# Optimization experiments

Hardware: AMD Instinct MI355X
Metric: run time of the kernel (lower is better)

## Reference

```python
import jax, jax.numpy as jnp
import numpy as np

T, B, D = 512, 16, 2048


def setup_inputs() -> dict:
    key = jax.random.key(0)
    k1, k2, k3, k4, k5 = jax.random.split(key, 5)
    scale = 1.0 / np.sqrt(D)  # keep tanh pre-activations in a sane range
    return {
        "h0": jax.random.normal(k1, (B, D), dtype=jnp.float32),
        "x": jax.random.normal(k2, (T, B, D), dtype=jnp.float32),
        "Wx": jax.random.normal(k3, (D, D), dtype=jnp.float32) * scale,
        "Wh": jax.random.normal(k4, (D, D), dtype=jnp.float32) * scale,
        "Wo": jax.random.normal(k5, (D, D), dtype=jnp.float32) * scale,
    }


def reference(h0, x, Wx, Wh, Wo):
    # ONNX Scan with 1 state var, 1 scan input (axis 0, forward direction),
    # 1 scan output (stacked on axis 0, forward direction), 3 outer vars.
    # Body: h' = tanh(x_t @ Wx + h @ Wh); y_t = h' @ Wo
    def step(h, x_t):
        h_new = jnp.tanh(x_t @ Wx + h @ Wh)   # [B, D]
        y_t = h_new @ Wo                      # [B, D]
        return h_new, y_t

    h_final, ys = jax.lax.scan(step, h0, x)   # ys: [T, B, D]
    return (h_final, ys)
```

## Files before the change

### kernel.cpp

```cpp
#include <hip/hip_runtime.h>
#include <hip/hip_bf16.h>

#define DD 2048
#define TT 512
#define NBLK 64
#define HF_SLOT 32768
#define KT 64
#define SENT32 0x7FC07FC0u

typedef __attribute__((ext_vector_type(4))) float  f32x4;
typedef __attribute__((ext_vector_type(8))) short  bf16x8;
typedef __attribute__((ext_vector_type(8))) unsigned short u16x8;
typedef unsigned short ushort_t;
typedef unsigned long long u64_t;

__device__ __forceinline__ void gld_lds16(const void* g, void* l) {
    __builtin_amdgcn_global_load_lds(
        (const __attribute__((address_space(1))) unsigned int*)g,
        (__attribute__((address_space(3))) unsigned int*)l, 16, 0, 0);
}

__device__ __forceinline__ ushort_t f2bf(float v) {
    __hip_bfloat16 h = __float2bfloat16(v);
    return *(ushort_t*)&h;
}

__device__ __forceinline__ u64_t llc_load64(const u64_t* p) {
    return __hip_atomic_load(p, __ATOMIC_RELAXED, __HIP_MEMORY_SCOPE_AGENT);
}
__device__ __forceinline__ void llc_store64(u64_t* p, u64_t v) {
    __hip_atomic_store(p, v, __ATOMIC_RELAXED, __HIP_MEMORY_SCOPE_AGENT);
}
__device__ __forceinline__ float llc_loadf(const float* p) {
    return __hip_atomic_load(p, __ATOMIC_RELAXED, __HIP_MEMORY_SCOPE_AGENT);
}

__global__ void conv_frag(const float* __restrict__ src, ushort_t* __restrict__ dst) {
    int id = blockIdx.x * 256 + threadIdx.x;
    int l  = id & 63;
    int sk = (id >> 6) & 63;
    int mt = id >> 12;
    const float* s = src + (size_t)(mt * 16 + (l & 15)) * DD + sk * 32 + ((l >> 4) * 8);
    float4 a = *(const float4*)s;
    float4 b = *(const float4*)(s + 4);
    u16x8 r;
    r[0] = f2bf(a.x); r[1] = f2bf(a.y); r[2] = f2bf(a.z); r[3] = f2bf(a.w);
    r[4] = f2bf(b.x); r[5] = f2bf(b.y); r[6] = f2bf(b.z); r[7] = f2bf(b.w);
    *(u16x8*)(dst + (size_t)id * 8) = r;
}

__global__ void conv_wt(const float* __restrict__ W, ushort_t* __restrict__ Wt) {
    int id = blockIdx.x * 256 + threadIdx.x;
    int n  = id & (DD - 1);
    int k8 = id >> 11;
    u16x8 r;
#pragma unroll
    for (int j = 0; j < 8; ++j)
        r[j] = f2bf(W[(size_t)(k8 * 8 + j) * DD + n]);
    *(u16x8*)(Wt + (size_t)n * DD + k8 * 8) = r;
}

__global__ void fill_sent(u64_t* __restrict__ dst) {
    size_t id = (size_t)blockIdx.x * 256 + threadIdx.x;
    u64_t v = 0x7FC07FC07FC07FC0ull;
    dst[id * 2]     = v;
    dst[id * 2 + 1] = v;
}

__global__ __launch_bounds__(256) void gemm_frag(
    const ushort_t* __restrict__ Af, const ushort_t* __restrict__ Bt,
    float* __restrict__ C) {
    __shared__ ushort_t lA[8 * 64 * 8];
    __shared__ ushort_t lB[8 * 64 * 8];
    int tid = threadIdx.x;
    int w = tid >> 6, l = tid & 63;
    int wm = w >> 1, wn = w & 1;
    int quad = l >> 4, col = l & 15;
    int mt0 = blockIdx.x * 8;
    int n0  = blockIdx.y * 128;

    f32x4 acc[4][4] = {};

    for (int sk = 0; sk < KT; ++sk) {
        __syncthreads();
#pragma unroll
        for (int q = 0; q < 2; ++q) {
            int i = w * 2 + q;
            const ushort_t* ga = Af + ((size_t)((mt0 + i) * 64 + sk) * 64 + l) * 8;
            gld_lds16(ga, &lA[i * 512]);
            int jt = i;
            const ushort_t* gb = Bt + (size_t)(n0 + jt * 16 + col) * DD + sk * 32 + quad * 8;
            gld_lds16(gb, &lB[jt * 512]);
        }
        __syncthreads();
        bf16x8 af[4], bf[4];
#pragma unroll
        for (int i = 0; i < 4; ++i) af[i] = *(const bf16x8*)&lA[((wm * 4 + i) * 64 + l) * 8];
#pragma unroll
        for (int j = 0; j < 4; ++j) bf[j] = *(const bf16x8*)&lB[((wn * 4 + j) * 64 + l) * 8];
#pragma unroll
        for (int i = 0; i < 4; ++i)
#pragma unroll
            for (int j = 0; j < 4; ++j)
                acc[i][j] = __builtin_amdgcn_mfma_f32_16x16x32_bf16(af[i], bf[j], acc[i][j], 0, 0, 0);
    }

#pragma unroll
    for (int i = 0; i < 4; ++i)
#pragma unroll
        for (int j = 0; j < 4; ++j) {
            int rg0 = (mt0 + wm * 4 + i) * 16 + quad * 4;
            int cg  = n0 + (wn * 4 + j) * 16 + col;
#pragma unroll
            for (int r = 0; r < 4; ++r)
                C[(size_t)(rg0 + r) * DD + cg] = acc[i][j][r];
        }
}

__global__ __launch_bounds__(256, 1) void rnn_fused(
    const ushort_t* __restrict__ Wht,
    const ushort_t* __restrict__ Wot,
    ushort_t* __restrict__ Hf,
    const float* __restrict__ A32,
    float* __restrict__ out) {
    __shared__ ushort_t lW[4 * 16 * 2 * 512];
    __shared__ float scr[2048];
    __shared__ ushort_t hstage[512];
    int tid = threadIdx.x;
    int w = tid >> 6, l = tid & 63;
    int quad = l >> 4, col = l & 15;
    bool is_rnn = blockIdx.x < NBLK;
    int b = is_rnn ? blockIdx.x : blockIdx.x - NBLK;
    int c0 = b * 32;
    float* ys = out + HF_SLOT;

    const ushort_t* Wsrc = is_rnn ? Wht : Wot;
#pragma unroll
    for (int s = 0; s < 16; ++s) {
        int sk = w * 16 + s;
#pragma unroll
        for (int jt = 0; jt < 2; ++jt) {
            const ushort_t* gb = Wsrc + (size_t)(c0 + jt * 16 + col) * DD + sk * 32 + quad * 8;
            gld_lds16(gb, &lW[((sk * 2 + jt) << 9)]);
        }
    }
    __syncthreads();

    for (int t = 1; t <= TT; ++t) {
        float av[4];
        if (is_rnn && w < 2) {
#pragma unroll
            for (int r = 0; r < 4; ++r)
                av[r] = llc_loadf(&A32[(size_t)((t - 1) * 16 + quad * 4 + r) * DD + c0 + w * 16 + col]);
        }

        const ushort_t* hsrc = Hf + (size_t)(is_rnn ? t - 1 : t) * HF_SLOT;
        const u64_t* hbase = (const u64_t*)hsrc + ((size_t)(w * 16) * 64 + l) * 2;

        f32x4 acc0 = {0.f, 0.f, 0.f, 0.f};
        f32x4 acc1 = {0.f, 0.f, 0.f, 0.f};
        unsigned pend = 0xFFFFu;
        while (pend) {
            u64_t q0[16], q1[16];
#pragma unroll
            for (int s = 0; s < 16; ++s)
                if (pend & (1u << s)) {
                    const u64_t* p = hbase + (size_t)s * 128;
                    q0[s] = llc_load64(p);
                    q1[s] = llc_load64(p + 1);
                }
#pragma unroll
            for (int s = 0; s < 16; ++s)
                if (pend & (1u << s)) {
                    unsigned x0 = (unsigned)q0[s], x1 = (unsigned)(q0[s] >> 32);
                    unsigned x2 = (unsigned)q1[s], x3 = (unsigned)(q1[s] >> 32);
                    bool ok = (x0 != SENT32) & (x1 != SENT32) & (x2 != SENT32) & (x3 != SENT32);
                    if (__all((int)ok)) {
                        pend &= ~(1u << s);
                        union { u64_t q[2]; bf16x8 v; } u;
                        u.q[0] = q0[s]; u.q[1] = q1[s];
                        int sk = w * 16 + s;
                        bf16x8 w0 = *(const bf16x8*)&lW[((sk * 2 + 0) << 9) + l * 8];
                        bf16x8 w1 = *(const bf16x8*)&lW[((sk * 2 + 1) << 9) + l * 8];
                        acc0 = __builtin_amdgcn_mfma_f32_16x16x32_bf16(u.v, w0, acc0, 0, 0, 0);
                        acc1 = __builtin_amdgcn_mfma_f32_16x16x32_bf16(u.v, w1, acc1, 0, 0, 0);
                    }
                }
        }

        *(f32x4*)&scr[((w * 2 + 0) * 64 + l) * 4] = acc0;
        *(f32x4*)&scr[((w * 2 + 1) * 64 + l) * 4] = acc1;
        __syncthreads();

        if (w < 2) {
            int jt = w;
            f32x4 p0 = *(f32x4*)&scr[((0 * 2 + jt) * 64 + l) * 4];
            f32x4 p1 = *(f32x4*)&scr[((1 * 2 + jt) * 64 + l) * 4];
            f32x4 p2 = *(f32x4*)&scr[((2 * 2 + jt) * 64 + l) * 4];
            f32x4 p3 = *(f32x4*)&scr[((3 * 2 + jt) * 64 + l) * 4];
            int lc = jt * 16 + col;
            if (is_rnn) {
                int q2 = lc >> 3, jj = lc & 7;
#pragma unroll
                for (int r = 0; r < 4; ++r) {
                    int m = quad * 4 + r;
                    float x = p0[r] + p1[r] + p2[r] + p3[r] + av[r];
                    float e2 = __expf(-2.f * fabsf(x));
                    float th = copysignf((1.f - e2) / (1.f + e2), x);
                    hstage[(q2 * 16 + m) * 8 + jj] = f2bf(th);
                    if (t == TT) out[(size_t)m * DD + c0 + lc] = th;
                }
            } else {
#pragma unroll
                for (int r = 0; r < 4; ++r) {
                    int m = quad * 4 + r;
                    float y = p0[r] + p1[r] + p2[r] + p3[r];
                    ys[(size_t)((t - 1) * 16 + m) * DD + c0 + lc] = y;
                }
            }
        }

        __syncthreads();

        if (is_rnn && w == 0) {
            u64_t* dst = (u64_t*)(Hf + (size_t)t * HF_SLOT + (size_t)(c0 >> 5) * 512);
            const u64_t* sp = (const u64_t*)hstage;
            llc_store64(dst + l,      sp[l]);
            llc_store64(dst + 64 + l, sp[64 + l]);
        }
    }
}

extern "C" void kernel_launch(void* const* d_in, const int* in_sizes, int n_in,
                              void* d_out, int out_size, void* d_ws, size_t ws_size,
                              hipStream_t stream) {
    const float* h0 = (const float*)d_in[0];
    const float* x  = (const float*)d_in[1];
    const float* Wx = (const float*)d_in[2];
    const float* Wh = (const float*)d_in[3];
    const float* Wo = (const float*)d_in[4];
    float* out = (float*)d_out;

    char* ws = (char*)d_ws;
    ushort_t* Hf  = (ushort_t*)(ws + 4096);
    ushort_t* Xf  = Hf + HF_SLOT;
    size_t hf_bytes = (size_t)(TT + 1) * HF_SLOT * 2;
    ushort_t* Wxt = (ushort_t*)(ws + 4096 + hf_bytes);
    ushort_t* Wht = Wxt + (size_t)DD * DD;
    ushort_t* Wot = Wht + (size_t)DD * DD;
    float* A32 = out + HF_SLOT;

    conv_frag<<<8192, 256, 0, stream>>>(x, Xf);
    conv_frag<<<16, 256, 0, stream>>>(h0, Hf);
    conv_wt<<<2048, 256, 0, stream>>>(Wx, Wxt);
    conv_wt<<<2048, 256, 0, stream>>>(Wh, Wht);
    conv_wt<<<2048, 256, 0, stream>>>(Wo, Wot);

    gemm_frag<<<dim3(64, 16), 256, 0, stream>>>(Xf, Wxt, A32);

    fill_sent<<<8192, 256, 0, stream>>>((u64_t*)(Hf + HF_SLOT));

    rnn_fused<<<2 * NBLK, 256, 0, stream>>>(Wht, Wot, Hf, A32, out);
}
```

Baseline: 2.377 ms.

## Add per-block step flags to gate hidden-state polling and split MFMA accumulators

Adds a per-block progress flag array in the workspace. Each consumer wave spins on one 32-bit flag per source block until it reaches the needed step, and only then issues the sentinel-checked loads of the hidden state. The hidden-state publish moves into the tanh waves right after staging, which drops one barrier-ordered store phase, and the flag store follows it. The MFMA accumulation is split into two independent chains per output tile to shorten the dependency chain. Flag polling adds extra atomic traffic, and the relaxed ordering between the data stores and the flag store relies on the sentinel checks that are still in place.

```diff
diff --git a/kernel.cpp b/kernel.cpp
--- a/kernel.cpp
+++ b/kernel.cpp
@@ -6,6 +6,7 @@
 #define NBLK 64
 #define HF_SLOT 32768
 #define KT 64
+#define FSTRIDE 16
 #define SENT32 0x7FC07FC0u
 
 typedef __attribute__((ext_vector_type(4))) float  f32x4;
@@ -30,6 +31,9 @@
 }
 __device__ __forceinline__ void llc_store64(u64_t* p, u64_t v) {
     __hip_atomic_store(p, v, __ATOMIC_RELAXED, __HIP_MEMORY_SCOPE_AGENT);
+}
+__device__ __forceinline__ unsigned llc_load32(const unsigned* p) {
+    return __hip_atomic_load(p, __ATOMIC_RELAXED, __HIP_MEMORY_SCOPE_AGENT);
 }
 __device__ __forceinline__ float llc_loadf(const float* p) {
     return __hip_atomic_load(p, __ATOMIC_RELAXED, __HIP_MEMORY_SCOPE_AGENT);
@@ -122,7 +126,8 @@
     const ushort_t* __restrict__ Wot,
     ushort_t* __restrict__ Hf,
     const float* __restrict__ A32,
-    float* __restrict__ out) {
+    float* __restrict__ out,
+    unsigned* __restrict__ flags) {
     __shared__ ushort_t lW[4 * 16 * 2 * 512];
     __shared__ float scr[2048];
     __shared__ ushort_t hstage[512];
@@ -146,6 +151,8 @@
     }
     __syncthreads();
 
+    const unsigned* fp = &flags[(w * 16 + (l & 15)) * FSTRIDE];
+
     for (int t = 1; t <= TT; ++t) {
         float av[4];
         if (is_rnn && w < 2) {
@@ -154,18 +161,24 @@
                 av[r] = llc_loadf(&A32[(size_t)((t - 1) * 16 + quad * 4 + r) * DD + c0 + w * 16 + col]);
         }
 
+        unsigned tgt = is_rnn ? (unsigned)(t - 1) : (unsigned)t;
+        {
+            unsigned f;
+            do { f = llc_load32(fp); } while (!__all((int)(f >= tgt)));
+        }
+
         const ushort_t* hsrc = Hf + (size_t)(is_rnn ? t - 1 : t) * HF_SLOT;
-        const u64_t* hbase = (const u64_t*)hsrc + ((size_t)(w * 16) * 64 + l) * 2;
-
-        f32x4 acc0 = {0.f, 0.f, 0.f, 0.f};
-        f32x4 acc1 = {0.f, 0.f, 0.f, 0.f};
+        const u64_t* hq = (const u64_t*)hsrc + ((size_t)(w * 16) * 64 + l) * 2;
+
+        f32x4 aA0 = {0.f,0.f,0.f,0.f}, aA1 = {0.f,0.f,0.f,0.f};
+        f32x4 aB0 = {0.f,0.f,0.f,0.f}, aB1 = {0.f,0.f,0.f,0.f};
         unsigned pend = 0xFFFFu;
+        u64_t q0[16], q1[16];
         while (pend) {
-            u64_t q0[16], q1[16];
 #pragma unroll
             for (int s = 0; s < 16; ++s)
                 if (pend & (1u << s)) {
-                    const u64_t* p = hbase + (size_t)s * 128;
+                    const u64_t* p = hq + (size_t)s * 128;
                     q0[s] = llc_load64(p);
                     q1[s] = llc_load64(p + 1);
                 }
@@ -182,11 +195,18 @@
                         int sk = w * 16 + s;
                         bf16x8 w0 = *(const bf16x8*)&lW[((sk * 2 + 0) << 9) + l * 8];
                         bf16x8 w1 = *(const bf16x8*)&lW[((sk * 2 + 1) << 9) + l * 8];
-                        acc0 = __builtin_amdgcn_mfma_f32_16x16x32_bf16(u.v, w0, acc0, 0, 0, 0);
-                        acc1 = __builtin_amdgcn_mfma_f32_16x16x32_bf16(u.v, w1, acc1, 0, 0, 0);
+                        if (s < 8) {
+                            aA0 = __builtin_amdgcn_mfma_f32_16x16x32_bf16(u.v, w0, aA0, 0, 0, 0);
+                            aA1 = __builtin_amdgcn_mfma_f32_16x16x32_bf16(u.v, w1, aA1, 0, 0, 0);
+                        } else {
+                            aB0 = __builtin_amdgcn_mfma_f32_16x16x32_bf16(u.v, w0, aB0, 0, 0, 0);
+                            aB1 = __builtin_amdgcn_mfma_f32_16x16x32_bf16(u.v, w1, aB1, 0, 0, 0);
+                        }
                     }
                 }
         }
+        f32x4 acc0 = aA0 + aB0;
+        f32x4 acc1 = aA1 + aB1;
 
         *(f32x4*)&scr[((w * 2 + 0) * 64 + l) * 4] = acc0;
         *(f32x4*)&scr[((w * 2 + 1) * 64 + l) * 4] = acc1;
@@ -210,6 +230,13 @@
                     hstage[(q2 * 16 + m) * 8 + jj] = f2bf(th);
                     if (t == TT) out[(size_t)m * DD + c0 + lc] = th;
                 }
+                asm volatile("s_waitcnt lgkmcnt(0)" ::: "memory");
+                u64_t v = ((const u64_t*)hstage)[w * 64 + l];
+                u64_t* dq = (u64_t*)(Hf + (size_t)t * HF_SLOT + (size_t)b * 512);
+                llc_store64(dq + w * 64 + l, v);
+                if (w == 0 && l == 0)
+                    __hip_atomic_store(&flags[b * FSTRIDE], (unsigned)t,
+                                       __ATOMIC_RELAXED, __HIP_MEMORY_SCOPE_AGENT);
             } else {
 #pragma unroll
                 for (int r = 0; r < 4; ++r) {
@@ -221,13 +248,6 @@
         }
 
         __syncthreads();
-
-        if (is_rnn && w == 0) {
-            u64_t* dst = (u64_t*)(Hf + (size_t)t * HF_SLOT + (size_t)(c0 >> 5) * 512);
-            const u64_t* sp = (const u64_t*)hstage;
-            llc_store64(dst + l,      sp[l]);
-            llc_store64(dst + 64 + l, sp[64 + l]);
-        }
     }
 }
 
@@ -242,6 +262,7 @@
     float* out = (float*)d_out;
 
     char* ws = (char*)d_ws;
+    unsigned* flags = (unsigned*)ws;
     ushort_t* Hf  = (ushort_t*)(ws + 4096);
     ushort_t* Xf  = Hf + HF_SLOT;
     size_t hf_bytes = (size_t)(TT + 1) * HF_SLOT * 2;
@@ -250,6 +271,8 @@
     ushort_t* Wot = Wht + (size_t)DD * DD;
     float* A32 = out + HF_SLOT;
 
+    hipMemsetAsync(d_ws, 0, 4096, stream);
+
     conv_frag<<<8192, 256, 0, stream>>>(x, Xf);
     conv_frag<<<16, 256, 0, stream>>>(h0, Hf);
     conv_wt<<<2048, 256, 0, stream>>>(Wx, Wxt);
@@ -260,5 +283,5 @@
 
     fill_sent<<<8192, 256, 0, stream>>>((u64_t*)(Hf + HF_SLOT));
 
-    rnn_fused<<<2 * NBLK, 256, 0, stream>>>(Wht, Wot, Hf, A32, out);
-}
+    rnn_fused<<<2 * NBLK, 256, 0, stream>>>(Wht, Wot, Hf, A32, out, flags);
+}
```

Result: slower. 2.714 ms (+14.2%).
